# Kernel optimization log

Hardware: AMD Instinct MI355X
Metric: run time of the kernel (lower is better)

Reference implementation:

```python
import jax, jax.numpy as jnp
import numpy as np

HIDDEN = 64
N_NODES = 100000
N_GRAPHS = 512


def setup_inputs() -> dict:
    key = jax.random.key(0)
    ks = jax.random.split(key, 16)
    N, E, G = N_NODES, 1600000, N_GRAPHS
    x = jax.random.normal(ks[0], (N, 1), dtype=jnp.float32)
    edge_index = jax.random.randint(ks[1], (2, E), 0, N, dtype=jnp.int64)
    batch = jnp.sort(jax.random.randint(ks[2], (N,), 0, G, dtype=jnp.int64))
    dist = jax.random.normal(ks[3], (G, 1), dtype=jnp.float32)
    sw = jax.random.normal(ks[4], (G, 1), dtype=jnp.float32)
    def lin(k, fan_in, fan_out):
        bound = 1.0 / np.sqrt(fan_in)
        kw, kb = jax.random.split(k)
        W = jax.random.uniform(kw, (fan_in, fan_out), minval=-bound, maxval=bound, dtype=jnp.float32)
        b = jax.random.uniform(kb, (fan_out,), minval=-bound, maxval=bound, dtype=jnp.float32)
        return W, b
    W1, b1 = lin(ks[5], 1, HIDDEN)
    W2, b2 = lin(ks[6], HIDDEN, HIDDEN)
    W3, b3 = lin(ks[7], HIDDEN, HIDDEN)
    Wl, bl = lin(ks[8], HIDDEN, 5)
    Wl1, bl1 = lin(ks[9], 7, 5)
    Wl2, bl2 = lin(ks[10], 5, 1)
    return dict(x=x, edge_index=edge_index, batch=batch, dist=dist, sw=sw,
                W1=W1, b1=b1, W2=W2, b2=b2, W3=W3, b3=b3,
                Wl=Wl, bl=bl, Wl1=Wl1, bl1=bl1, Wl2=Wl2, bl2=bl2)


def _gcn_conv(x, W, b, src, dst, norm, num_nodes):
    # x @ W, gather source features per edge, weight by sym-norm, scatter-add to target
    h = x @ W  # [N, out]
    msg = h[src] * norm[:, None]  # [E', out]
    out = jax.ops.segment_sum(msg, dst, num_segments=num_nodes)
    return out + b


def reference(x, edge_index, batch, dist, sw, W1, b1, W2, b2, W3, b3, Wl, bl, Wl1, bl1, Wl2, bl2):
    N = x.shape[0]
    G = dist.shape[0]
    # add self-loops (PyG GCNConv default)
    loop = jnp.arange(N, dtype=edge_index.dtype)
    src = jnp.concatenate([edge_index[0], loop])
    dst = jnp.concatenate([edge_index[1], loop])
    # symmetric gcn_norm: deg over target index, norm = d^-1/2[src] * d^-1/2[dst]
    deg = jax.ops.segment_sum(jnp.ones_like(src, dtype=x.dtype), dst, num_segments=N)
    dinv = jnp.where(deg > 0, jax.lax.rsqrt(jnp.maximum(deg, 1.0)), 0.0)
    norm = dinv[src] * dinv[dst]

    h = jax.nn.relu(_gcn_conv(x, W1, b1, src, dst, norm, N))
    h = jax.nn.relu(_gcn_conv(h, W2, b2, src, dst, norm, N))
    h = _gcn_conv(h, W3, b3, src, dst, norm, N)

    # global_mean_pool over graph ids
    sums = jax.ops.segment_sum(h, batch, num_segments=G)
    cnts = jax.ops.segment_sum(jnp.ones((N,), dtype=h.dtype), batch, num_segments=G)
    pooled = sums / jnp.maximum(cnts, 1.0)[:, None]

    # dropout is identity in eval mode
    g = pooled @ Wl + bl  # [G, 5]
    g = jnp.concatenate([g, dist, sw], axis=1)  # [G, 7]
    g = jax.nn.relu(g @ Wl1 + bl1)
    return g @ Wl2 + bl2  # [G, 1]
```

## Files before the change

### kernel.cpp

```cpp
#include <hip/hip_runtime.h>
#include <hip/hip_bf16.h>

#define HID 64
#define WPAD 68
#define NXCD 8

typedef float v2f __attribute__((ext_vector_type(2)));

static __device__ __forceinline__ float bflo(unsigned u) { return __uint_as_float(u << 16); }
static __device__ __forceinline__ float bfhi(unsigned u) {
    return __uint_as_float(u & 0xFFFF0000u);
}
static __device__ __forceinline__ unsigned packbf(float a, float b) {
    __hip_bfloat16 ha = __float2bfloat16(a), hb = __float2bfloat16(b);
    unsigned short ua = *reinterpret_cast<unsigned short*>(&ha);
    unsigned short ub = *reinterpret_cast<unsigned short*>(&hb);
    return (unsigned)ua | ((unsigned)ub << 16);
}


__global__ __launch_bounds__(256) void fill_part(const int* __restrict__ ei, int E, int N,
                                                 int* __restrict__ cnt, int* __restrict__ csr) {
    int xcd = blockIdx.x & (NXCD - 1);
    int sl = blockIdx.x >> 3;
    int nsl = gridDim.x >> 3;
    int nlo = (int)((long long)N * xcd / NXCD);
    int nhi = (int)((long long)N * (xcd + 1) / NXCD);
    int stride = nsl * blockDim.x;
    int tid = sl * blockDim.x + threadIdx.x;
    for (int eb = tid; eb < E; eb += stride * 4) {
        int dd[4], ss[4];
#pragma unroll
        for (int u = 0; u < 4; u++) {
            int e = eb + u * stride;
            bool ok = e < E;
            dd[u] = ok ? ei[E + e] : -1;
            ss[u] = ok ? ei[e] : 0;
        }
#pragma unroll
        for (int u = 0; u < 4; u++) {
            int d = dd[u];
            if (d >= nlo && d < nhi) {
                int pos = atomicAdd(&cnt[d], 1);
                csr[(d << 6) + pos] = ss[u];
            }
        }
    }
}

__global__ void prep_kernel(const int* __restrict__ cnt, const float* __restrict__ x,
                            const int* __restrict__ batch, int4* __restrict__ rec,
                            float* __restrict__ xs, uint2* __restrict__ padA,
                            uint2* __restrict__ padB, int N) {
    int gid = blockIdx.x * blockDim.x + threadIdx.x;
    if (gid < 16) {
        padA[gid] = make_uint2(0u, 0u);
        padB[gid] = make_uint2(0u, 0u);
    }
    int stride = gridDim.x * blockDim.x;
    for (int n = gid; n < N; n += stride) {
        int deg = cnt[n];
        float dn = rsqrtf((float)(deg + 1));
        rec[n] = make_int4(deg, __float_as_int(dn), batch[n], 0);
        xs[n] = dn * x[n];
    }
}

__global__ void bounds_kernel(const int* __restrict__ batch, int* __restrict__ gb, int N, int G) {
    int n = blockIdx.x * blockDim.x + threadIdx.x;
    if (n >= N) return;
    int b = batch[n];
    if (n == 0) {
        for (int g = 0; g <= b; g++) gb[g] = 0;
    } else {
        int pb = batch[n - 1];
        for (int g = pb + 1; g <= b; g++) gb[g] = n;
    }
    if (n == N - 1) {
        for (int g = b + 1; g <= G; g++) gb[g] = N;
    }
}


__global__ void table_kernel(const float* __restrict__ W1, const float* __restrict__ b1,
                             const float* __restrict__ W2, float* __restrict__ tsort,
                             float* __restrict__ tabA, float* __restrict__ tabB) {
    int j = threadIdx.x;
    float a = W1[j], b = b1[j];
    float t = (a != 0.f) ? (-b / a) : 3.4e38f;
    int rank = 0;
#pragma unroll 8
    for (int k = 0; k < 64; k++) {
        float tk = __shfl(t, k);
        rank += (tk < t) || (tk == t && k < j);
    }
    __shared__ float st[64];
    __shared__ int sperm[64];
    st[rank] = t;
    sperm[rank] = j;
    __syncthreads();
    tsort[j] = st[j];
    int f = j;
    float A = 0.f, B = 0.f;
#pragma unroll 4
    for (int k = 0; k < 64; k++) {
        float ak = W1[k], bk = b1[k], w = W2[k * 64 + f];
        if (ak < 0.f) { A += ak * w; B += bk * w; }
        else if (ak == 0.f && bk > 0.f) { B += bk * w; }
    }
    tabA[f] = A;
    tabB[f] = B;
#pragma unroll 4
    for (int s = 1; s <= 64; s++) {
        int jj = sperm[s - 1];
        float aj = W1[jj], bj = b1[jj], w = W2[jj * 64 + f];
        if (aj > 0.f) { A += aj * w; B += bj * w; }
        else if (aj < 0.f) { A -= aj * w; B -= bj * w; }
        tabA[s * 64 + f] = A;
        tabB[s * 64 + f] = B;
    }
}


__device__ __forceinline__ void stageW(const float* __restrict__ W, float* __restrict__ sW) {
    for (int i = threadIdx.x; i < HID * HID; i += 256) {
        int r = i >> 6, c = i & 63;
        sW[r * WPAD + c] = W[i];
    }
    __syncthreads();
}

__device__ __forceinline__ void qmatmul(float4 h4, const float* __restrict__ sW, int q, int sl,
                                        v2f& z0, v2f& z1) {
    z0 = (v2f){0.f, 0.f};
    z1 = (v2f){0.f, 0.f};
#pragma unroll
    for (int t = 0; t < 16; t++) {
        int k = (q << 4) + t;
        int srclane = 20 * q + (t >> 2);
        float comp = ((t & 3) == 0) ? h4.x : ((t & 3) == 1) ? h4.y : ((t & 3) == 2) ? h4.z : h4.w;
        float hk = __shfl(comp, srclane);
        const v2f* w2 = reinterpret_cast<const v2f*>(&sW[k * WPAD + sl * 4]);
        z0 += hk * w2[0];
        z1 += hk * w2[1];
    }
#pragma unroll
    for (int off = 16; off <= 32; off <<= 1) {
        z0.x += __shfl_xor(z0.x, off);
        z0.y += __shfl_xor(z0.y, off);
        z1.x += __shfl_xor(z1.x, off);
        z1.y += __shfl_xor(z1.y, off);
    }
}


__global__ __launch_bounds__(256) void layer1_kernel(
    const float* __restrict__ xs, const int* __restrict__ csr, const int4* __restrict__ rec,
    const float* __restrict__ tsort, const float* __restrict__ tabA,
    const float* __restrict__ tabB, char* __restrict__ zb, int N) {
    int lane = threadIdx.x & 63;
    float tl = tsort[lane];
    int n = blockIdx.x * 4 + (threadIdx.x >> 6);
    if (n >= N) return;
    const int4 r = rec[n];
    float dn = __int_as_float(r.y);
    float acc = (lane < r.x) ? xs[csr[(n << 6) + lane]] : 0.f;
#pragma unroll
    for (int off = 32; off; off >>= 1) acc += __shfl_xor(acc, off);
    float p = dn * (acc + xs[n]);
    int s = __popcll(__ballot(tl <= p));
    float zf = dn * (p * tabA[s * 64 + lane] + tabB[s * 64 + lane]);
    float zo = __shfl_xor(zf, 1);
    if (!(lane & 1))
        *reinterpret_cast<unsigned*>(zb + (((size_t)n) << 7) + ((lane >> 1) << 2)) =
            packbf(zf, zo);
}


template <bool FUSE, bool POOL>
__global__ __launch_bounds__(256) void p64_kernel(
    const char* __restrict__ zbase, const int* __restrict__ csr, const int4* __restrict__ rec,
    const float* __restrict__ bias, const float* __restrict__ W,
    uint2* __restrict__ outb, float* __restrict__ outp, int N) {
    __shared__ float sW[FUSE ? HID * WPAD : 1];
    __shared__ float pbuf[POOL ? 16 : 1][POOL ? HID : 1];
    __shared__ int pg[16];
    if (FUSE) stageW(W, sW);
    int lane = threadIdx.x & 63;
    int wid = threadIdx.x >> 6;
    int q = lane >> 4, sl = lane & 15;
    int n0 = blockIdx.x * 16 + wid * 4;
    if (!POOL && n0 >= N) return;
    unsigned soff = (unsigned)(sl << 3);

    int deg[4], bat[4], ew[4], mt[4], ncl[4];
    float dn[4];
    int mtmax = 0;
#pragma unroll
    for (int k = 0; k < 4; k++) {
        int n = n0 + k;
        bool v = n < N;
        ncl[k] = v ? n : N;
        const int4 r = rec[v ? n : 0];
        deg[k] = v ? r.x : 0;
        dn[k] = __int_as_float(r.y);
        bat[k] = v ? r.z : -1;
        ew[k] = (lane < deg[k]) ? csr[((v ? n : 0) << 6) + lane] : N;
        mt[k] = (deg[k] + 3) >> 2;
        mtmax = max(mtmax, mt[k]);
    }
    v2f a0[4], a1[4];
#pragma unroll
    for (int k = 0; k < 4; k++) {
        a0[k] = (v2f){0.f, 0.f};
        a1[k] = (v2f){0.f, 0.f};
    }
    for (int tb = 0; tb < mtmax; tb += 4) {
#pragma unroll
        for (int u = 0; u < 4; u++) {
            int t = tb + u;
            int eidx = ((t << 2) + q) & 63;
#pragma unroll
            for (int k = 0; k < 4; k++) {
                int ss = __shfl(ew[k], eidx);
                ss = (t < mt[k]) ? ss : N;
                const uint2 rr = *reinterpret_cast<const uint2*>(
                    zbase + (((unsigned)ss << 7) + soff));
                v2f u0 = {bflo(rr.x), bfhi(rr.x)};
                v2f u1 = {bflo(rr.y), bfhi(rr.y)};
                a0[k] += u0;
                a1[k] += u1;
            }
        }
    }
    const float4 b4 = *reinterpret_cast<const float4*>(&bias[sl << 2]);
#pragma unroll
    for (int k = 0; k < 4; k++) {
#pragma unroll
        for (int off = 16; off <= 32; off <<= 1) {
            a0[k].x += __shfl_xor(a0[k].x, off);
            a0[k].y += __shfl_xor(a0[k].y, off);
            a1[k].x += __shfl_xor(a1[k].x, off);
            a1[k].y += __shfl_xor(a1[k].y, off);
        }
        const uint2 su = *reinterpret_cast<const uint2*>(
            zbase + (((unsigned)ncl[k] << 7) + soff));
        a0[k].x = dn[k] * (a0[k].x + bflo(su.x));
        a0[k].y = dn[k] * (a0[k].y + bfhi(su.x));
        a1[k].x = dn[k] * (a1[k].x + bflo(su.y));
        a1[k].y = dn[k] * (a1[k].y + bfhi(su.y));
    }

    if (FUSE) {
#pragma unroll
        for (int k = 0; k < 4; k++) {
            float4 h;
            h.x = fmaxf(a0[k].x + b4.x, 0.f);
            h.y = fmaxf(a0[k].y + b4.y, 0.f);
            h.z = fmaxf(a1[k].x + b4.z, 0.f);
            h.w = fmaxf(a1[k].y + b4.w, 0.f);
            v2f z0, z1;
            qmatmul(h, sW, q, sl, z0, z1);
            if (q == 0 && n0 + k < N)
                outb[(size_t)(n0 + k) * 16 + sl] =
                    make_uint2(packbf(dn[k] * z0.x, dn[k] * z0.y),
                               packbf(dn[k] * z1.x, dn[k] * z1.y));
        }
    } else if (POOL) {
        if (q == 0) {
#pragma unroll
            for (int k = 0; k < 4; k++) {
                *reinterpret_cast<float4*>(&pbuf[wid * 4 + k][sl << 2]) =
                    make_float4(a0[k].x + b4.x, a0[k].y + b4.y, a1[k].x + b4.z, a1[k].y + b4.w);
                if (sl == 0) pg[wid * 4 + k] = bat[k];
            }
        }
        __syncthreads();
        if (wid == 0) {
            int j = lane;
            float v = 0.f;
            int gp = -1;
#pragma unroll
            for (int w = 0; w < 16; w++) {
                int gw = pg[w];
                if (gw < 0) continue;
                if (gw == gp) {
                    v += pbuf[w][j];
                } else {
                    if (gp >= 0) atomicAdd(&outp[(size_t)gp * HID + j], v);
                    v = pbuf[w][j];
                    gp = gw;
                }
            }
            if (gp >= 0) atomicAdd(&outp[(size_t)gp * HID + j], v);
        }
    }
}


__global__ void head_kernel(const float* __restrict__ psum, const int* __restrict__ gb,
                            const float* __restrict__ dist, const float* __restrict__ sw,
                            const float* __restrict__ Wl, const float* __restrict__ bl,
                            const float* __restrict__ Wl1, const float* __restrict__ bl1,
                            const float* __restrict__ Wl2, const float* __restrict__ bl2,
                            float* __restrict__ out, int G) {
    int g = blockIdx.x * blockDim.x + threadIdx.x;
    if (g >= G) return;
    int c = gb[g + 1] - gb[g];
    float invc = 1.f / fmaxf((float)c, 1.f);
    float a[5];
#pragma unroll
    for (int k = 0; k < 5; k++) a[k] = bl[k];
    for (int j = 0; j < HID; j++) {
        float p = psum[(size_t)g * HID + j] * invc;
#pragma unroll
        for (int k = 0; k < 5; k++) a[k] += p * Wl[j * 5 + k];
    }
    float g7[7];
#pragma unroll
    for (int k = 0; k < 5; k++) g7[k] = a[k];
    g7[5] = dist[g];
    g7[6] = sw[g];
    float r = bl2[0];
#pragma unroll
    for (int k2 = 0; k2 < 5; k2++) {
        float t = bl1[k2];
#pragma unroll
        for (int j = 0; j < 7; j++) t += g7[j] * Wl1[j * 5 + k2];
        t = fmaxf(t, 0.f);
        r += t * Wl2[k2];
    }
    out[g] = r;
}


extern "C" void kernel_launch(void* const* d_in, const int* in_sizes, int n_in,
                              void* d_out, int out_size, void* d_ws, size_t ws_size,
                              hipStream_t stream) {
    const float* x    = (const float*)d_in[0];
    const int*   ei   = (const int*)d_in[1];
    const int*   batch= (const int*)d_in[2];
    const float* dist = (const float*)d_in[3];
    const float* sw   = (const float*)d_in[4];
    const float* W1   = (const float*)d_in[5];
    const float* b1   = (const float*)d_in[6];
    const float* W2   = (const float*)d_in[7];
    const float* b2   = (const float*)d_in[8];
    const float* W3   = (const float*)d_in[9];
    const float* b3   = (const float*)d_in[10];
    const float* Wl   = (const float*)d_in[11];
    const float* bl   = (const float*)d_in[12];
    const float* Wl1  = (const float*)d_in[13];
    const float* bl1  = (const float*)d_in[14];
    const float* Wl2  = (const float*)d_in[15];
    const float* bl2  = (const float*)d_in[16];

    int N = in_sizes[0];
    int E = in_sizes[1] / 2;
    int G = in_sizes[3];

    char* ws = (char*)d_ws;
    size_t off = 0;
    auto alloc = [&](size_t bytes) -> char* {
        char* p = ws + off;
        off += (bytes + 255) & ~(size_t)255;
        return p;
    };
    char*  zreg      = ws;
    int*   cnt       = (int*)alloc((size_t)N * 4);
    float* psum      = (float*)alloc((size_t)G * HID * 4);
    size_t zbytes    = off;
    int4*  rec       = (int4*)alloc((size_t)N * 16);
    float* xs        = (float*)alloc((size_t)N * 4);
    int*   gb        = (int*)alloc(((size_t)G + 1) * 4);
    float* tsort     = (float*)alloc(64 * 4);
    float* tabA      = (float*)alloc(65 * 64 * 4);
    float* tabB      = (float*)alloc(65 * 64 * 4);
    char*  bufA      = alloc(((size_t)N + 1) * 128);
    char*  bufB      = alloc(((size_t)N + 1) * 128);
    int*   csr       = (int*)alloc((size_t)N * 64 * 4);

    hipMemsetAsync(zreg, 0, zbytes, stream);

    table_kernel<<<1, 64, 0, stream>>>(W1, b1, W2, tsort, tabA, tabB);
    fill_part<<<2048, 256, 0, stream>>>(ei, E, N, cnt, csr);
    prep_kernel<<<(N + 255) / 256, 256, 0, stream>>>(
        cnt, x, batch, rec, xs,
        (uint2*)(bufA + (size_t)N * 128), (uint2*)(bufB + (size_t)N * 128), N);
    bounds_kernel<<<(N + 255) / 256, 256, 0, stream>>>(batch, gb, N, G);

    int nb1 = (N + 3) / 4;
    int nb4 = (N + 15) / 16;
    layer1_kernel<<<nb1, 256, 0, stream>>>(xs, csr, rec, tsort, tabA, tabB, bufA, N);
    p64_kernel<true, false><<<nb4, 256, 0, stream>>>(bufA, csr, rec, b2, W3,
                                                     (uint2*)bufB, nullptr, N);
    p64_kernel<false, true><<<nb4, 256, 0, stream>>>(bufB, csr, rec, b3, nullptr,
                                                     nullptr, psum, N);
    head_kernel<<<(G + 255) / 256, 256, 0, stream>>>(psum, gb, dist, sw, Wl, bl, Wl1, bl1, Wl2,
                                                     bl2, (float*)d_out, G);
}
```

Before: 265.6 us.

## Vectorize edge-index loads in CSR fill and cut registers in aggregation kernel

The CSR fill kernel now reads destination and source indices as int4 vectors when E is a multiple of 4, replacing strided scalar loads, with a scalar fallback otherwise. The p64 aggregation kernel gains a min-blocks-per-SM launch bound of 8. It also stops keeping per-node degree, norm, batch and clamp arrays live across the gather loop, reloading them from rec afterwards. This lowers register pressure to allow higher occupancy, at the cost of extra small reloads and possible spills under the tighter bound.

```diff
diff --git a/kernel.cpp b/kernel.cpp
--- a/kernel.cpp
+++ b/kernel.cpp
@@ -28,21 +28,30 @@
     int nhi = (int)((long long)N * (xcd + 1) / NXCD);
     int stride = nsl * blockDim.x;
     int tid = sl * blockDim.x + threadIdx.x;
-    for (int eb = tid; eb < E; eb += stride * 4) {
-        int dd[4], ss[4];
-#pragma unroll
-        for (int u = 0; u < 4; u++) {
-            int e = eb + u * stride;
-            bool ok = e < E;
-            dd[u] = ok ? ei[E + e] : -1;
-            ss[u] = ok ? ei[e] : 0;
-        }
-#pragma unroll
-        for (int u = 0; u < 4; u++) {
-            int d = dd[u];
+    if ((E & 3) == 0) {
+        const int4* d4p = reinterpret_cast<const int4*>(ei + E);
+        const int4* s4p = reinterpret_cast<const int4*>(ei);
+        int E4 = E >> 2;
+        for (int i = tid; i < E4; i += stride) {
+            int4 d4 = d4p[i];
+            int4 s4 = s4p[i];
+            int dd[4] = {d4.x, d4.y, d4.z, d4.w};
+            int ss[4] = {s4.x, s4.y, s4.z, s4.w};
+#pragma unroll
+            for (int u = 0; u < 4; u++) {
+                int d = dd[u];
+                if (d >= nlo && d < nhi) {
+                    int pos = atomicAdd(&cnt[d], 1);
+                    csr[(d << 6) + pos] = ss[u];
+                }
+            }
+        }
+    } else {
+        for (int e = tid; e < E; e += stride) {
+            int d = ei[E + e];
             if (d >= nlo && d < nhi) {
                 int pos = atomicAdd(&cnt[d], 1);
-                csr[(d << 6) + pos] = ss[u];
+                csr[(d << 6) + pos] = ei[e];
             }
         }
     }
@@ -178,7 +187,7 @@
 
 
 template <bool FUSE, bool POOL>
-__global__ __launch_bounds__(256) void p64_kernel(
+__global__ __launch_bounds__(256, 8) void p64_kernel(
     const char* __restrict__ zbase, const int* __restrict__ csr, const int4* __restrict__ rec,
     const float* __restrict__ bias, const float* __restrict__ W,
     uint2* __restrict__ outb, float* __restrict__ outp, int N) {
@@ -193,28 +202,19 @@
     if (!POOL && n0 >= N) return;
     unsigned soff = (unsigned)(sl << 3);
 
-    int deg[4], bat[4], ew[4], mt[4], ncl[4];
-    float dn[4];
-    int mtmax = 0;
+    int ew[4], mt[4];
+    v2f a0[4], a1[4];
 #pragma unroll
     for (int k = 0; k < 4; k++) {
         int n = n0 + k;
         bool v = n < N;
-        ncl[k] = v ? n : N;
-        const int4 r = rec[v ? n : 0];
-        deg[k] = v ? r.x : 0;
-        dn[k] = __int_as_float(r.y);
-        bat[k] = v ? r.z : -1;
-        ew[k] = (lane < deg[k]) ? csr[((v ? n : 0) << 6) + lane] : N;
-        mt[k] = (deg[k] + 3) >> 2;
-        mtmax = max(mtmax, mt[k]);
-    }
-    v2f a0[4], a1[4];
-#pragma unroll
-    for (int k = 0; k < 4; k++) {
+        int deg = v ? rec[n].x : 0;
+        ew[k] = (lane < deg) ? csr[((v ? n : 0) << 6) + lane] : N;
+        mt[k] = (deg + 3) >> 2;
         a0[k] = (v2f){0.f, 0.f};
         a1[k] = (v2f){0.f, 0.f};
     }
+    int mtmax = max(max(mt[0], mt[1]), max(mt[2], mt[3]));
     for (int tb = 0; tb < mtmax; tb += 4) {
 #pragma unroll
         for (int u = 0; u < 4; u++) {
@@ -243,17 +243,17 @@
             a1[k].x += __shfl_xor(a1[k].x, off);
             a1[k].y += __shfl_xor(a1[k].y, off);
         }
+        int n = n0 + k;
+        bool v = n < N;
+        float dnk = __int_as_float(rec[v ? n : 0].y);
         const uint2 su = *reinterpret_cast<const uint2*>(
-            zbase + (((unsigned)ncl[k] << 7) + soff));
-        a0[k].x = dn[k] * (a0[k].x + bflo(su.x));
-        a0[k].y = dn[k] * (a0[k].y + bfhi(su.x));
-        a1[k].x = dn[k] * (a1[k].x + bflo(su.y));
-        a1[k].y = dn[k] * (a1[k].y + bfhi(su.y));
-    }
-
-    if (FUSE) {
-#pragma unroll
-        for (int k = 0; k < 4; k++) {
+            zbase + (((unsigned)(v ? n : N) << 7) + soff));
+        a0[k].x = dnk * (a0[k].x + bflo(su.x));
+        a0[k].y = dnk * (a0[k].y + bfhi(su.x));
+        a1[k].x = dnk * (a1[k].x + bflo(su.y));
+        a1[k].y = dnk * (a1[k].y + bfhi(su.y));
+
+        if (FUSE) {
             float4 h;
             h.x = fmaxf(a0[k].x + b4.x, 0.f);
             h.y = fmaxf(a0[k].y + b4.y, 0.f);
@@ -261,18 +261,20 @@
             h.w = fmaxf(a1[k].y + b4.w, 0.f);
             v2f z0, z1;
             qmatmul(h, sW, q, sl, z0, z1);
-            if (q == 0 && n0 + k < N)
-                outb[(size_t)(n0 + k) * 16 + sl] =
-                    make_uint2(packbf(dn[k] * z0.x, dn[k] * z0.y),
-                               packbf(dn[k] * z1.x, dn[k] * z1.y));
-        }
-    } else if (POOL) {
+            if (q == 0 && v)
+                outb[(size_t)n * 16 + sl] = make_uint2(packbf(dnk * z0.x, dnk * z0.y),
+                                                       packbf(dnk * z1.x, dnk * z1.y));
+        }
+    }
+    if (POOL) {
         if (q == 0) {
 #pragma unroll
             for (int k = 0; k < 4; k++) {
+                int n = n0 + k;
+                bool v = n < N;
                 *reinterpret_cast<float4*>(&pbuf[wid * 4 + k][sl << 2]) =
                     make_float4(a0[k].x + b4.x, a0[k].y + b4.y, a1[k].x + b4.z, a1[k].y + b4.w);
-                if (sl == 0) pg[wid * 4 + k] = bat[k];
+                if (sl == 0) pg[wid * 4 + k] = v ? rec[n].z : -1;
             }
         }
         __syncthreads();
```

Result: slower. 408.6 us (+53.8%).
